# Kernel tuning notes

Measured on AMD Instinct MI355X. Metric: run time of the kernel, lower is better.

The kernel has to match this reference:

```python
import jax, jax.numpy as jnp
import numpy as np

N_TASK, N_RET, N_DRAM, N_LINK = 50000, 20000, 5000, 100000
E_RET, E_DRAM, E_LINK = 1_000_000, 250_000, 2_000_000
H = 64


def setup_inputs() -> dict:
    key = jax.random.key(0)
    k = jax.random.split(key, 17)
    s = 1.0 / np.sqrt(3 * H)
    return {
        "feat_ret":  jax.random.normal(k[0], (E_RET, 1), jnp.float32),
        "feat_dram": jax.random.normal(k[1], (E_DRAM, 1), jnp.float32),
        "feat_link": jax.random.normal(k[2], (E_LINK, 1), jnp.float32),
        "W_ret":  jax.random.normal(k[3], (H, 1), jnp.float32),
        "b_ret":  jax.random.normal(k[4], (H,), jnp.float32) * 0.1,
        "W_dram": jax.random.normal(k[5], (H, 1), jnp.float32),
        "b_dram": jax.random.normal(k[6], (H,), jnp.float32) * 0.1,
        "W_link": jax.random.normal(k[7], (H, 1), jnp.float32),
        "b_link": jax.random.normal(k[8], (H,), jnp.float32) * 0.1,
        "W_task": jax.random.normal(k[9], (H, 3 * H), jnp.float32) * s,
        "b_task": jax.random.normal(k[10], (H,), jnp.float32) * 0.1,
        "task_ret":  jax.random.randint(k[11], (E_RET,), 0, N_TASK),
        "mod_ret":   jax.random.randint(k[12], (E_RET,), 0, N_RET),
        "task_dram": jax.random.randint(k[13], (E_DRAM,), 0, N_TASK),
        "mod_dram":  jax.random.randint(k[14], (E_DRAM,), 0, N_DRAM),
        "task_link": jax.random.randint(k[15], (E_LINK,), 0, N_TASK),
        "mod_link":  jax.random.randint(k[16], (E_LINK,), 0, N_LINK),
    }


def _gather_inp(feat, mod_idx, n_mod, W, b):
    # use_X: copy_e('feat') + sum per module node, then Linear(1,H) + tanh (activate_inp)
    inp = jax.ops.segment_sum(feat, mod_idx, num_segments=n_mod)  # [n_mod, 1]
    return jnp.tanh(inp @ W.T + b)                                # [n_mod, H]


def _max_to_task(inp_mod, mod_idx, task_idx, n_task):
    # X_used_by: copy_u('inp') + max per task node; zero-in-degree tasks -> 0 (DGL convention)
    m = jax.ops.segment_max(inp_mod[mod_idx], task_idx, num_segments=n_task)
    deg = jax.ops.segment_sum(jnp.ones_like(task_idx), task_idx, num_segments=n_task)
    return jnp.where((deg > 0)[:, None], m, 0.0)


def reference(feat_ret, feat_dram, feat_link, W_ret, b_ret, W_dram, b_dram,
              W_link, b_link, W_task, b_task,
              task_ret, mod_ret, task_dram, mod_dram, task_link, mod_link):
    # _module_update_inp
    inp_ret  = _gather_inp(feat_ret,  mod_ret,  N_RET,  W_ret,  b_ret)
    inp_dram = _gather_inp(feat_dram, mod_dram, N_DRAM, W_dram, b_dram)
    inp_link = _gather_inp(feat_link, mod_link, N_LINK, W_link, b_link)

    # _task_update_h: per-etype max reduce, cross-etype concat, Linear(3H,H) + tanh
    h_cat = jnp.concatenate([
        _max_to_task(inp_ret,  mod_ret,  task_ret,  N_TASK),
        _max_to_task(inp_dram, mod_dram, task_dram, N_TASK),
        _max_to_task(inp_link, mod_link, task_link, N_TASK),
    ], axis=-1)                                                   # [N_TASK, 3H]
    h_task = jnp.tanh(h_cat @ W_task.T + b_task)                  # [N_TASK, H]

    # _module_update_h: use_link copy_u('h') + mean per link node
    s = jax.ops.segment_sum(h_task[task_link], mod_link, num_segments=N_LINK)
    deg = jax.ops.segment_sum(jnp.ones((E_LINK,), jnp.float32), mod_link, num_segments=N_LINK)
    h_link = jnp.where((deg > 0)[:, None], s / jnp.maximum(deg, 1.0)[:, None], 0.0)
    return h_link
```

## Files before the change

### kernel.cpp

```cpp
#include <hip/hip_runtime.h>
#include <stdint.h>

#define N_TASK 50000
#define N_RET 20000
#define N_DRAM 5000
#define N_LINK 100000
#define E_RET 1000000
#define E_DRAM 250000
#define E_LINK 2000000

#define SBE 4096
#define NS_RET 245
#define NS_DRAM 62
#define NS_LINK 489
#define NS_TOT (NS_RET + NS_DRAM + NS_LINK)
#define MR_RET 64
#define RSZ_RET 313
#define MR_DRAM 16
#define RSZ_DRAM 313
#define MR_LINK 256
#define RSZ_LINK 391
#define RECIP313 107203u
#define RECIP391 85817u
#define CAPM_RET 16250
#define CAPM_DRAM 16250
#define CAPM_LINK 8255
#define BM4_RET 0
#define BM4_DRAM (MR_RET * NS_RET)
#define BM4_LINK (BM4_DRAM + MR_DRAM * NS_DRAM)
#define BM4_TOT (BM4_LINK + MR_LINK * NS_LINK)
#define BT_RET 0
#define BT_DRAM (16 * NS_RET)
#define BT_LINK (BT_DRAM + 16 * NS_DRAM)
#define BT_TOT (BT_LINK + 16 * NS_LINK)

#define R_PART 3125
#define CAP_RET 63800
#define CAP_DRAM 16300
#define CAP_LINK 126800
#define SUB_RET 4
#define SUB_DRAM 1
#define SUB_LINK 8
#define PB_RET 0
#define PB_DRAM (16 * SUB_RET * R_PART)
#define PB_LINK (PB_DRAM + 16 * SUB_DRAM * R_PART)
#define PB_TOT (PB_LINK + 16 * SUB_LINK * R_PART)

#define WS_SRET 0
#define WS_SDRAM 80000
#define WS_SLINK 100000
#define WS_CNT 500000
#define WS_OFFS 900000
#define WS_TMAX 1300000
#define WS_TMIN 1900000
#define WS_BCNT 2500000
#define WS_RCNT 2500192
#define WS_CSR 2501536
#define WS_BLKM 10501536
#define WS_BLKB 11068960
#define WS_MREC_RET 15701536
#define WS_MREC_DRAM 24021536
#define WS_MREC_LINK 26101536
#define WS_PART1 15701536
#define WS_HPL0_1 20901536
#define WS_HPL1_1 24101536
#define WS_TREC32_RET 43007776
#define WS_TREC32_DRAM 47090976
#define WS_TREC32_LINK 48134176
#define WS_WTB_1 56249376
#define WS_NEED1 56273952
#define WS_PART2 10501536
#define WS_TREC_RET 15701536
#define WS_TREC_DRAM 23867936
#define WS_TREC_LINK 25954336
#define WS_HPL0_2 15701536
#define WS_HPL1_2 18901536
#define WS_WTB_2 43007776
#define WS_NEED2 43032352

typedef __attribute__((ext_vector_type(8))) short bf16x8;
typedef __attribute__((ext_vector_type(4))) float f32x4;
typedef unsigned long long u64;

__device__ __forceinline__ unsigned ford(float f) {
  unsigned u = __float_as_uint(f);
  return (u & 0x80000000u) ? ~u : (u | 0x80000000u);
}
__device__ __forceinline__ float funord(unsigned t) {
  unsigned u = (t & 0x80000000u) ? (t & 0x7fffffffu) : ~t;
  return __uint_as_float(u);
}
__device__ __forceinline__ unsigned short bf16rne(float f) {
  unsigned u = __float_as_uint(f);
  return (unsigned short)((u + 0x7fffu + ((u >> 16) & 1u)) >> 16);
}

__device__ __forceinline__ void decode_sblk(int bx, int& e, int& blk, int& E0, int& NB,
                                            int& NR, unsigned& RECIP, int& RSZ, int& base) {
  if (bx < NS_RET) {
    e = 0; blk = bx; E0 = E_RET; NB = NS_RET; NR = MR_RET; RECIP = RECIP313; RSZ = RSZ_RET; base = BM4_RET;
  } else if (bx < NS_RET + NS_DRAM) {
    e = 1; blk = bx - NS_RET; E0 = E_DRAM; NB = NS_DRAM; NR = MR_DRAM; RECIP = RECIP313; RSZ = RSZ_DRAM; base = BM4_DRAM;
  } else {
    e = 2; blk = bx - NS_RET - NS_DRAM; E0 = E_LINK; NB = NS_LINK; NR = MR_LINK; RECIP = RECIP391; RSZ = RSZ_LINK; base = BM4_LINK;
  }
}
__device__ __forceinline__ void decode_stblk(int bx, int& e, int& blk, int& E0, int& NB,
                                             int& baset) {
  if (bx < NS_RET) { e = 0; blk = bx; E0 = E_RET; NB = NS_RET; baset = BT_RET; }
  else if (bx < NS_RET + NS_DRAM) { e = 1; blk = bx - NS_RET; E0 = E_DRAM; NB = NS_DRAM; baset = BT_DRAM; }
  else { e = 2; blk = bx - NS_RET - NS_DRAM; E0 = E_LINK; NB = NS_LINK; baset = BT_LINK; }
}


__global__ __launch_bounds__(256) void k_count3(
    const int* __restrict__ mr, const int* __restrict__ md, const int* __restrict__ ml,
    const float* __restrict__ W_task, unsigned short* __restrict__ wtb,
    int* __restrict__ blkcnt_m, int* __restrict__ tcur) {
  int bx = blockIdx.x, tid = threadIdx.x;
  if (bx == NS_TOT + 48) {
    if (tid < 48) tcur[tid] = 0;
    return;
  }
  if (bx >= NS_TOT) {
    int i = (bx - NS_TOT) * 256 + tid;
    if (i < 64 * 192) wtb[i] = bf16rne(W_task[i]);
    return;
  }
  __shared__ int c[256];
  int e, blk, E0, NB, NR, RSZ, base; unsigned RECIP;
  decode_sblk(bx, e, blk, E0, NB, NR, RECIP, RSZ, base);
  const int* mod = (e == 0) ? mr : (e == 1) ? md : ml;
  c[tid] = 0;
  __syncthreads();
  int i0 = blk * SBE;
#pragma unroll
  for (int q = 0; q < 16; q++) {
    int i = i0 + q * 256 + tid;
    if (i < E0) {
      int m = mod[i];
      int r = (int)(((u64)(unsigned)m * RECIP) >> 25);
      atomicAdd(&c[r], 1);
    }
  }
  __syncthreads();
  for (int r = tid; r < NR; r += 256)
    blkcnt_m[base + r * NB + blk] = c[r];
}

__global__ __launch_bounds__(512) void k_scan3(const int* __restrict__ blkcnt_m,
                                               int* __restrict__ blkbase_m,
                                               int* __restrict__ rcnt) {
  __shared__ int sm[512];
  int gb = blockIdx.x, tid = threadIdx.x;
  int NB, off;
  if (gb < 64) { NB = NS_RET; off = BM4_RET + gb * NS_RET; }
  else if (gb < 80) { NB = NS_DRAM; off = BM4_DRAM + (gb - 64) * NS_DRAM; }
  else { NB = NS_LINK; off = BM4_LINK + (gb - 80) * NS_LINK; }
  int v = (tid < NB) ? blkcnt_m[off + tid] : 0;
  sm[tid] = v;
  __syncthreads();
  for (int d = 1; d < 512; d <<= 1) {
    int x = (tid >= d) ? sm[tid - d] : 0;
    __syncthreads();
    sm[tid] += x;
    __syncthreads();
  }
  if (tid < NB) blkbase_m[off + tid] = sm[tid] - v;
  if (tid == 511) rcnt[gb] = sm[511];
}

__global__ __launch_bounds__(512) void k_mscatter3(
    const int* __restrict__ mr, const int* __restrict__ md, const int* __restrict__ ml,
    const int* __restrict__ tr, const int* __restrict__ td, const int* __restrict__ tl,
    const float* __restrict__ fr, const float* __restrict__ fd, const float* __restrict__ fl,
    const int* __restrict__ blkcnt_m, const int* __restrict__ blkbase_m,
    u64* __restrict__ mrec_ret, u64* __restrict__ mrec_dram, u64* __restrict__ mrec_link) {
  __shared__ int lcur[256];
  __shared__ int pdelta[256];
  __shared__ int sscan[256];
  __shared__ u64 srec[SBE];
  __shared__ int sdelta[SBE];
  int tid = threadIdx.x;
  int e, blk, E0, NB, NR, RSZ, base; unsigned RECIP;
  decode_sblk(blockIdx.x, e, blk, E0, NB, NR, RECIP, RSZ, base);
  const int* mod = (e == 0) ? mr : (e == 1) ? md : ml;
  const int* task = (e == 0) ? tr : (e == 1) ? td : tl;
  const float* feat = (e == 0) ? fr : (e == 1) ? fd : fl;
  u64* out = (e == 0) ? mrec_ret : (e == 1) ? mrec_dram : mrec_link;
  int CAP = (e == 0) ? CAPM_RET : (e == 1) ? CAPM_DRAM : CAPM_LINK;
  int cnt_r = 0, base_r = 0;
  if (tid < NR) {
    cnt_r = blkcnt_m[base + tid * NB + blk];
    base_r = blkbase_m[base + tid * NB + blk];
  }
  if (tid < 256) sscan[tid] = cnt_r;
  __syncthreads();
  for (int d = 1; d < 256; d <<= 1) {
    int x = (tid < 256 && tid >= d) ? sscan[tid - d] : 0;
    __syncthreads();
    if (tid < 256) sscan[tid] += x;
    __syncthreads();
  }
  if (tid < 256) {
    int excl = sscan[tid] - cnt_r;
    lcur[tid] = excl;
    pdelta[tid] = tid * CAP + base_r - excl;
  }
  __syncthreads();
  int i0 = blk * SBE;
#pragma unroll
  for (int q = 0; q < 8; q++) {
    int i = i0 + q * 512 + tid;
    if (i < E0) {
      int m = mod[i];
      int r = (int)(((u64)(unsigned)m * RECIP) >> 25);
      unsigned mloc = (unsigned)(m - r * RSZ);
      unsigned tk = (unsigned)task[i];
      unsigned fu = __float_as_uint(feat[i]);
      int slot = atomicAdd(&lcur[r], 1);
      srec[slot] = ((u64)fu << 32) | (tk << 16) | mloc;
      int gpos = pdelta[r] + slot - r * CAP;
      sdelta[slot] = (gpos < CAP) ? pdelta[r] : (int)0x80000000;
    }
  }
  __syncthreads();
  int total = E0 - i0; if (total > SBE) total = SBE;
  for (int s = tid; s < total; s += 512) {
    int d = sdelta[s];
    if (d != (int)0x80000000) out[d + s] = srec[s];
  }
}

__global__ __launch_bounds__(1024) void k_msum3(
    const u64* __restrict__ mrec_ret, const u64* __restrict__ mrec_dram,
    const u64* __restrict__ mrec_link, const int* __restrict__ rcnt,
    int* __restrict__ cnt, int* __restrict__ offs, int* __restrict__ csr,
    int* __restrict__ tcur,
    unsigned* __restrict__ trec_ret, unsigned* __restrict__ trec_dram,
    unsigned* __restrict__ trec_link) {
  __shared__ float ssum[RSZ_LINK];
  __shared__ int scnt[RSZ_LINK];
  __shared__ int soff[RSZ_LINK + 1];
  __shared__ int red[512];
  __shared__ int tcnt16[16][16];
  __shared__ int tbase16[16][16];
  int gb = blockIdx.x, tid = threadIdx.x;
  int w = tid >> 6;
  int e, rl, RSZ, CAPM, Ntot, CAPT;
  const u64* p;
  unsigned* trec;
  if (gb < MR_RET) {
    e = 0; rl = gb; p = mrec_ret + (long)rl * CAPM_RET;
    RSZ = RSZ_RET; CAPM = CAPM_RET; Ntot = N_RET; CAPT = CAP_RET; trec = trec_ret;
  } else if (gb < MR_RET + MR_DRAM) {
    e = 1; rl = gb - MR_RET; p = mrec_dram + (long)rl * CAPM_DRAM;
    RSZ = RSZ_DRAM; CAPM = CAPM_DRAM; Ntot = N_DRAM; CAPT = CAP_DRAM; trec = trec_dram;
  } else {
    e = 2; rl = gb - MR_RET - MR_DRAM; p = mrec_link + (long)rl * CAPM_LINK;
    RSZ = RSZ_LINK; CAPM = CAPM_LINK; Ntot = N_LINK; CAPT = CAP_LINK; trec = trec_link;
  }
  int m0 = rl * RSZ;
  int nmod = Ntot - m0; if (nmod > RSZ) nmod = RSZ;
  for (int j = tid; j < RSZ; j += 1024) { ssum[j] = 0.f; scnt[j] = 0; }
  if (tid < 256) tcnt16[tid >> 4][tid & 15] = 0;
  __syncthreads();
  int count = rcnt[gb]; if (count > CAPM) count = CAPM;
  for (int i = tid; i < count; i += 1024) {
    u64 rec = p[i];
    int mloc = (int)(rec & 0xFFFFull);
    int task = (int)((rec >> 16) & 0xFFFFull);
    atomicAdd(&ssum[mloc], __uint_as_float((unsigned)(rec >> 32)));
    if (e == 2) atomicAdd(&scnt[mloc], 1);
    atomicAdd(&tcnt16[w][task / R_PART], 1);
  }
  __syncthreads();
  if (tid < 16) {
    int b2 = tid, tot = 0;
    for (int w2 = 0; w2 < 16; w2++) { tbase16[w2][b2] = tot; tot += tcnt16[w2][b2]; }
    int g0 = atomicAdd(&tcur[e * 16 + b2], tot);
    for (int w2 = 0; w2 < 16; w2++) { tbase16[w2][b2] += g0; tcnt16[w2][b2] = 0; }
  }
  if (e == 2) {
    int partial = (tid < 256 && 80 + tid < gb) ? rcnt[80 + tid] : 0;
    if (tid < 256) red[tid] = partial;
    __syncthreads();
    for (int s = 128; s > 0; s >>= 1) {
      if (tid < s) red[tid] += red[tid + s];
      __syncthreads();
    }
    int rb = red[0];
    __syncthreads();
    int vv = (tid < 512 && tid < nmod) ? scnt[tid] : 0;
    if (tid < 512) red[tid] = vv;
    __syncthreads();
    for (int d = 1; d < 512; d <<= 1) {
      int x = (tid < 512 && tid >= d) ? red[tid - d] : 0;
      __syncthreads();
      if (tid < 512) red[tid] += x;
      __syncthreads();
    }
    if (tid < nmod) soff[tid] = red[tid] - vv;
    __syncthreads();
    for (int j = tid; j < nmod; j += 1024) {
      cnt[m0 + j] = scnt[j];
      offs[m0 + j] = rb + soff[j];
    }
    __syncthreads();
    for (int i = tid; i < count; i += 1024) {
      u64 rec = p[i];
      int mloc = (int)(rec & 0xFFFFull);
      int task = (int)((rec >> 16) & 0xFFFFull);
      int lp = atomicAdd(&soff[mloc], 1);
      csr[rb + lp] = task;
    }
  }
  __syncthreads();
  for (int i = tid; i < count; i += 1024) {
    u64 rec = p[i];
    int mloc = (int)(rec & 0xFFFFull);
    int task = (int)((rec >> 16) & 0xFFFFull);
    int b = task / R_PART;
    unsigned tl12 = (unsigned)(task - b * R_PART);
    unsigned u = (ford(ssum[mloc]) & 0xFFFFF000u) | tl12;
    int local = atomicAdd(&tcnt16[w][b], 1);
    int pos = tbase16[w][b] + local;
    if (pos < CAPT) trec[(long)b * CAPT + pos] = u;
  }
}

__global__ __launch_bounds__(256) void k_passb3(
    const unsigned* __restrict__ trec_ret, const unsigned* __restrict__ trec_dram,
    const unsigned* __restrict__ trec_link,
    const int* __restrict__ tcur, unsigned* __restrict__ partials) {
  __shared__ unsigned lmax[R_PART];
  __shared__ unsigned lmin[R_PART];
  int blk = blockIdx.x;
  int e, b, sub, Nb, PB, CAP;
  const unsigned* bkt;
  if (blk < 16 * SUB_RET) {
    e = 0; b = blk >> 2; sub = blk & 3; Nb = SUB_RET; PB = PB_RET; CAP = CAP_RET; bkt = trec_ret;
  } else if (blk < 16 * (SUB_RET + SUB_DRAM)) {
    int q = blk - 16 * SUB_RET;
    e = 1; b = q; sub = 0; Nb = SUB_DRAM; PB = PB_DRAM; CAP = CAP_DRAM; bkt = trec_dram;
  } else {
    int q = blk - 16 * (SUB_RET + SUB_DRAM);
    e = 2; b = q >> 3; sub = q & 7; Nb = SUB_LINK; PB = PB_LINK; CAP = CAP_LINK; bkt = trec_link;
  }
  for (int idx = threadIdx.x; idx < R_PART; idx += 256) {
    lmax[idx] = 0u;
    lmin[idx] = 0xFFFFFFFFu;
  }
  __syncthreads();
  int count = tcur[e * 16 + b];
  if (count > CAP) count = CAP;
  int chunk = (count + Nb - 1) / Nb;
  int s0 = sub * chunk;
  int s1 = s0 + chunk; if (s1 > count) s1 = count;
  const unsigned* p = bkt + (long)b * CAP;
  for (int i = s0 + threadIdx.x; i < s1; i += 256) {
    unsigned rec = p[i];
    unsigned r = rec & 0xFFFu;
    atomicMax(&lmax[r], rec);
    atomicMin(&lmin[r], rec);
  }
  __syncthreads();
  unsigned gbase = PB + (unsigned)(b * Nb + sub) * R_PART;
  for (int idx = threadIdx.x; idx < R_PART; idx += 256) {
    partials[gbase + idx] = lmax[idx];
    partials[PB_TOT + gbase + idx] = lmin[idx];
  }
}

__global__ __launch_bounds__(256) void k_mmred3(const unsigned* __restrict__ partials,
                                                unsigned* __restrict__ tmax,
                                                unsigned* __restrict__ tmin) {
  int gid = blockIdx.x * 256 + threadIdx.x;
  if (gid >= 3 * N_TASK) return;
  int e = gid / N_TASK;
  int t = gid - e * N_TASK;
  int Nb = (e == 0) ? SUB_RET : (e == 1) ? SUB_DRAM : SUB_LINK;
  int PB = (e == 0) ? PB_RET : (e == 1) ? PB_DRAM : PB_LINK;
  int b = t / R_PART;
  int r = t - b * R_PART;
  unsigned umax = 0u, umin = 0xFFFFFFFFu;
  for (int sub = 0; sub < Nb; sub++) {
    unsigned idx = PB + (unsigned)(b * Nb + sub) * R_PART + r;
    unsigned wv = partials[idx];
    if (wv > umax) umax = wv;
    unsigned w2 = partials[PB_TOT + idx];
    if (w2 < umin) umin = w2;
  }
  tmax[gid] = umax & 0xFFFFF000u;
  tmin[gid] = umin & 0xFFFFF000u;
}


__global__ __launch_bounds__(256) void k_count(
    const int* __restrict__ mr, const int* __restrict__ md, const int* __restrict__ ml,
    const int* __restrict__ tr, const int* __restrict__ td, const int* __restrict__ tl,
    const float* __restrict__ W_task, unsigned short* __restrict__ wtb,
    int* __restrict__ blkcnt_m, int* __restrict__ blkcnt_t) {
  int bx = blockIdx.x, tid = threadIdx.x;
  if (bx >= 2 * NS_TOT) {
    int i = (bx - 2 * NS_TOT) * 256 + tid;
    if (i < 64 * 192) wtb[i] = bf16rne(W_task[i]);
    return;
  }
  __shared__ int c[256];
  c[tid] = 0;
  __syncthreads();
  if (bx < NS_TOT) {
    int e, blk, E0, NB, NR, RSZ, base; unsigned RECIP;
    decode_sblk(bx, e, blk, E0, NB, NR, RECIP, RSZ, base);
    const int* mod = (e == 0) ? mr : (e == 1) ? md : ml;
    int i0 = blk * SBE;
#pragma unroll
    for (int q = 0; q < 16; q++) {
      int i = i0 + q * 256 + tid;
      if (i < E0) {
        int m = mod[i];
        int r = (int)(((u64)(unsigned)m * RECIP) >> 25);
        atomicAdd(&c[r], 1);
      }
    }
    __syncthreads();
    for (int r = tid; r < NR; r += 256)
      blkcnt_m[base + r * NB + blk] = c[r];
  } else {
    int e, blk, E0, NB, baset;
    decode_stblk(bx - NS_TOT, e, blk, E0, NB, baset);
    const int* task = (e == 0) ? tr : (e == 1) ? td : tl;
    int i0 = blk * SBE;
#pragma unroll
    for (int q = 0; q < 16; q++) {
      int i = i0 + q * 256 + tid;
      if (i < E0) atomicAdd(&c[task[i] / R_PART], 1);
    }
    __syncthreads();
    if (tid < 16) blkcnt_t[baset + tid * NB + blk] = c[tid];
  }
}

__global__ __launch_bounds__(512) void k_scan(int* __restrict__ blkcnt_m,
                                              int* __restrict__ blkcnt_t,
                                              int* __restrict__ rcnt, int* __restrict__ bcnt) {
  __shared__ int sm[512];
  int gb = blockIdx.x, tid = threadIdx.x;
  int* arr; int NB; int* outp;
  if (gb < 336) {
    int off;
    if (gb < 64) { NB = NS_RET; off = BM4_RET + gb * NS_RET; }
    else if (gb < 80) { NB = NS_DRAM; off = BM4_DRAM + (gb - 64) * NS_DRAM; }
    else { NB = NS_LINK; off = BM4_LINK + (gb - 80) * NS_LINK; }
    arr = blkcnt_m + off; outp = rcnt + gb;
  } else {
    int g = gb - 336; int e = g >> 4, b = g & 15;
    int NBe = (e == 0) ? NS_RET : (e == 1) ? NS_DRAM : NS_LINK;
    int baset = (e == 0) ? BT_RET : (e == 1) ? BT_DRAM : BT_LINK;
    NB = NBe; arr = blkcnt_t + baset + b * NBe; outp = bcnt + g;
  }
  int v = (tid < NB) ? arr[tid] : 0;
  sm[tid] = v;
  __syncthreads();
  for (int d = 1; d < 512; d <<= 1) {
    int x = (tid >= d) ? sm[tid - d] : 0;
    __syncthreads();
    sm[tid] += x;
    __syncthreads();
  }
  if (tid < NB) arr[tid] = sm[tid] - v;
  if (tid == 511) *outp = sm[511];
}

__global__ __launch_bounds__(256) void k_mscatter2(
    const int* __restrict__ mr, const int* __restrict__ md, const int* __restrict__ ml,
    const int* __restrict__ tl,
    const float* __restrict__ fr, const float* __restrict__ fd, const float* __restrict__ fl,
    const int* __restrict__ blkcnt_m,
    u64* __restrict__ mrec_ret, u64* __restrict__ mrec_dram, u64* __restrict__ mrec_link) {
  __shared__ int lcur[256];
  __shared__ int pdelta[256];
  __shared__ int sscan[256];
  __shared__ u64 srec[SBE];
  __shared__ int sdelta[SBE];
  int tid = threadIdx.x;
  int e, blk, E0, NB, NR, RSZ, base; unsigned RECIP;
  decode_sblk(blockIdx.x, e, blk, E0, NB, NR, RECIP, RSZ, base);
  const int* mod = (e == 0) ? mr : (e == 1) ? md : ml;
  const float* feat = (e == 0) ? fr : (e == 1) ? fd : fl;
  u64* out = (e == 0) ? mrec_ret : (e == 1) ? mrec_dram : mrec_link;
  int CAP = (e == 0) ? CAPM_RET : (e == 1) ? CAPM_DRAM : CAPM_LINK;
  lcur[tid] = 0;
  __syncthreads();
  int i0 = blk * SBE;
#pragma unroll
  for (int q = 0; q < 16; q++) {
    int i = i0 + q * 256 + tid;
    if (i < E0) {
      int m = mod[i];
      int r = (int)(((u64)(unsigned)m * RECIP) >> 25);
      atomicAdd(&lcur[r], 1);
    }
  }
  __syncthreads();
  int v = lcur[tid];
  sscan[tid] = v;
  __syncthreads();
  for (int d = 1; d < 256; d <<= 1) {
    int x = (tid >= d) ? sscan[tid - d] : 0;
    __syncthreads();
    sscan[tid] += x;
    __syncthreads();
  }
  int excl = sscan[tid] - v;
  int total = sscan[255];
  int gbv = (tid < NR) ? blkcnt_m[base + tid * NB + blk] : 0;
  __syncthreads();
  lcur[tid] = excl;
  pdelta[tid] = tid * CAP + gbv - excl;
  __syncthreads();
#pragma unroll
  for (int q = 0; q < 16; q++) {
    int i = i0 + q * 256 + tid;
    if (i < E0) {
      int m = mod[i];
      int r = (int)(((u64)(unsigned)m * RECIP) >> 25);
      unsigned mloc = (unsigned)(m - r * RSZ);
      unsigned task = (e == 2) ? (unsigned)tl[i] : 0u;
      unsigned fu = __float_as_uint(feat[i]);
      int slot = atomicAdd(&lcur[r], 1);
      srec[slot] = ((u64)fu << 32) | (task << 16) | mloc;
      int gpos = pdelta[r] + slot - r * CAP;
      sdelta[slot] = (gpos < CAP) ? pdelta[r] : (int)0x80000000;
    }
  }
  __syncthreads();
  for (int s = tid; s < total; s += 256) {
    int d = sdelta[s];
    if (d != (int)0x80000000) out[d + s] = srec[s];
  }
}

__global__ __launch_bounds__(256) void k_msum(
    const u64* __restrict__ mrec_ret, const u64* __restrict__ mrec_dram,
    const u64* __restrict__ mrec_link, const int* __restrict__ rcnt,
    float* __restrict__ s_ret, float* __restrict__ s_dram, float* __restrict__ s_link,
    int* __restrict__ cnt, int* __restrict__ offs, int* __restrict__ csr) {
  __shared__ float ssum[RSZ_LINK];
  __shared__ int scnt[RSZ_LINK];
  __shared__ int soff[RSZ_LINK + 1];
  __shared__ int red[256];
  int gb = blockIdx.x, tid = threadIdx.x;
  int e, rl, RSZ, CAP, Ntot;
  const u64* p;
  float* sout;
  if (gb < MR_RET) {
    e = 0; rl = gb; p = mrec_ret + (long)rl * CAPM_RET; sout = s_ret;
    RSZ = RSZ_RET; CAP = CAPM_RET; Ntot = N_RET;
  } else if (gb < MR_RET + MR_DRAM) {
    e = 1; rl = gb - MR_RET; p = mrec_dram + (long)rl * CAPM_DRAM; sout = s_dram;
    RSZ = RSZ_DRAM; CAP = CAPM_DRAM; Ntot = N_DRAM;
  } else {
    e = 2; rl = gb - MR_RET - MR_DRAM; p = mrec_link + (long)rl * CAPM_LINK; sout = s_link;
    RSZ = RSZ_LINK; CAP = CAPM_LINK; Ntot = N_LINK;
  }
  int m0 = rl * RSZ;
  int nmod = Ntot - m0; if (nmod > RSZ) nmod = RSZ;
  for (int j = tid; j < RSZ; j += 256) { ssum[j] = 0.f; scnt[j] = 0; }
  __syncthreads();
  int count = rcnt[gb]; if (count > CAP) count = CAP;
  for (int i = tid; i < count; i += 256) {
    u64 rec = p[i];
    int mloc = (int)(rec & 0xFFFFull);
    atomicAdd(&ssum[mloc], __uint_as_float((unsigned)(rec >> 32)));
    if (e == 2) atomicAdd(&scnt[mloc], 1);
  }
  __syncthreads();
  for (int j = tid; j < nmod; j += 256) sout[m0 + j] = ssum[j];
  if (e != 2) return;
  int partial = (80 + tid < gb) ? rcnt[80 + tid] : 0;
  red[tid] = partial;
  __syncthreads();
  for (int s = 128; s > 0; s >>= 1) {
    if (tid < s) red[tid] += red[tid + s];
    __syncthreads();
  }
  int rb = red[0];
  __syncthreads();
  int a0 = (2 * tid < nmod) ? scnt[2 * tid] : 0;
  int a1 = (2 * tid + 1 < nmod) ? scnt[2 * tid + 1] : 0;
  red[tid] = a0 + a1;
  __syncthreads();
  for (int d = 1; d < 256; d <<= 1) {
    int x = (tid >= d) ? red[tid - d] : 0;
    __syncthreads();
    red[tid] += x;
    __syncthreads();
  }
  int excl = red[tid] - (a0 + a1);
  if (2 * tid < RSZ_LINK) soff[2 * tid] = excl;
  if (2 * tid + 1 < RSZ_LINK) soff[2 * tid + 1] = excl + a0;
  __syncthreads();
  for (int j = tid; j < nmod; j += 256) {
    cnt[m0 + j] = scnt[j];
    offs[m0 + j] = rb + soff[j];
  }
  __syncthreads();
  for (int i = tid; i < count; i += 256) {
    u64 rec = p[i];
    int mloc = (int)(rec & 0xFFFFull);
    int task = (int)((rec >> 16) & 0xFFFFull);
    int lp = atomicAdd(&soff[mloc], 1);
    csr[rb + lp] = task;
  }
}

__global__ __launch_bounds__(256) void k_ascatter2(
    const int* __restrict__ tr, const int* __restrict__ mr,
    const int* __restrict__ td, const int* __restrict__ md,
    const int* __restrict__ tl, const int* __restrict__ ml,
    const float* __restrict__ s_ret, const float* __restrict__ s_dram,
    const float* __restrict__ s_link, const int* __restrict__ blkcnt_t,
    u64* __restrict__ trec_ret, u64* __restrict__ trec_dram, u64* __restrict__ trec_link) {
  __shared__ int lcur[256];
  __shared__ int pdelta[256];
  __shared__ int sscan[256];
  __shared__ u64 srec[SBE];
  __shared__ int sdelta[SBE];
  int tid = threadIdx.x;
  int e, blk, E0, NB, baset;
  decode_stblk(blockIdx.x, e, blk, E0, NB, baset);
  const int* task = (e == 0) ? tr : (e == 1) ? td : tl;
  const int* mod = (e == 0) ? mr : (e == 1) ? md : ml;
  const float* s = (e == 0) ? s_ret : (e == 1) ? s_dram : s_link;
  u64* out = (e == 0) ? trec_ret : (e == 1) ? trec_dram : trec_link;
  int CAP = (e == 0) ? CAP_RET : (e == 1) ? CAP_DRAM : CAP_LINK;
  lcur[tid] = 0;
  __syncthreads();
  int i0 = blk * SBE;
#pragma unroll
  for (int q = 0; q < 16; q++) {
    int i = i0 + q * 256 + tid;
    if (i < E0) atomicAdd(&lcur[task[i] / R_PART], 1);
  }
  __syncthreads();
  int v = lcur[tid];
  sscan[tid] = v;
  __syncthreads();
  for (int d = 1; d < 256; d <<= 1) {
    int x = (tid >= d) ? sscan[tid - d] : 0;
    __syncthreads();
    sscan[tid] += x;
    __syncthreads();
  }
  int excl = sscan[tid] - v;
  int total = sscan[255];
  int gbv = (tid < 16) ? blkcnt_t[baset + tid * NB + blk] : 0;
  __syncthreads();
  lcur[tid] = excl;
  pdelta[tid] = tid * CAP + gbv - excl;
  __syncthreads();
#pragma unroll
  for (int q = 0; q < 16; q++) {
    int i = i0 + q * 256 + tid;
    if (i < E0) {
      int t = task[i];
      int r = t / R_PART;
      unsigned rloc = (unsigned)(t - r * R_PART);
      unsigned u = ford(s[mod[i]]);
      int slot = atomicAdd(&lcur[r], 1);
      srec[slot] = ((u64)u << 32) | rloc;
      int gpos = pdelta[r] + slot - r * CAP;
      sdelta[slot] = (gpos < CAP) ? pdelta[r] : (int)0x80000000;
    }
  }
  __syncthreads();
  for (int sidx = tid; sidx < total; sidx += 256) {
    int d = sdelta[sidx];
    if (d != (int)0x80000000) out[d + sidx] = srec[sidx];
  }
}

__global__ __launch_bounds__(256) void k_passb(
    const u64* __restrict__ trec_ret, const u64* __restrict__ trec_dram,
    const u64* __restrict__ trec_link,
    const int* __restrict__ bcnt, unsigned* __restrict__ partials) {
  __shared__ unsigned lmax[R_PART];
  __shared__ unsigned lmin[R_PART];
  int blk = blockIdx.x;
  int e, b, sub, Nb, PB, CAP;
  const u64* bkt;
  if (blk < 16 * SUB_RET) {
    e = 0; b = blk >> 2; sub = blk & 3; Nb = SUB_RET; PB = PB_RET; CAP = CAP_RET; bkt = trec_ret;
  } else if (blk < 16 * (SUB_RET + SUB_DRAM)) {
    int q = blk - 16 * SUB_RET;
    e = 1; b = q; sub = 0; Nb = SUB_DRAM; PB = PB_DRAM; CAP = CAP_DRAM; bkt = trec_dram;
  } else {
    int q = blk - 16 * (SUB_RET + SUB_DRAM);
    e = 2; b = q >> 3; sub = q & 7; Nb = SUB_LINK; PB = PB_LINK; CAP = CAP_LINK; bkt = trec_link;
  }
  for (int idx = threadIdx.x; idx < R_PART; idx += 256) {
    lmax[idx] = 0u;
    lmin[idx] = 0xFFFFFFFFu;
  }
  __syncthreads();
  int count = bcnt[e * 16 + b];
  if (count > CAP) count = CAP;
  int chunk = (count + Nb - 1) / Nb;
  int s0 = sub * chunk;
  int s1 = s0 + chunk; if (s1 > count) s1 = count;
  const u64* p = bkt + (long)b * CAP;
  for (int i = s0 + threadIdx.x; i < s1; i += 256) {
    u64 rec = p[i];
    unsigned r = (unsigned)rec;
    unsigned u = (unsigned)(rec >> 32);
    atomicMax(&lmax[r], u);
    atomicMin(&lmin[r], u);
  }
  __syncthreads();
  unsigned gbase = PB + (unsigned)(b * Nb + sub) * R_PART;
  for (int idx = threadIdx.x; idx < R_PART; idx += 256) {
    partials[gbase + idx] = lmax[idx];
    partials[PB_TOT + gbase + idx] = lmin[idx];
  }
}

__global__ __launch_bounds__(256) void k_mmred2(const unsigned* __restrict__ partials,
                                                unsigned* __restrict__ tmax,
                                                unsigned* __restrict__ tmin) {
  int gid = blockIdx.x * 256 + threadIdx.x;
  if (gid >= 3 * N_TASK) return;
  int e = gid / N_TASK;
  int t = gid - e * N_TASK;
  int Nb = (e == 0) ? SUB_RET : (e == 1) ? SUB_DRAM : SUB_LINK;
  int PB = (e == 0) ? PB_RET : (e == 1) ? PB_DRAM : PB_LINK;
  int b = t / R_PART;
  int r = t - b * R_PART;
  unsigned umax = 0u, umin = 0xFFFFFFFFu;
  for (int sub = 0; sub < Nb; sub++) {
    unsigned idx = PB + (unsigned)(b * Nb + sub) * R_PART + r;
    unsigned wv = partials[idx];
    if (wv > umax) umax = wv;
    unsigned w2 = partials[PB_TOT + idx];
    if (w2 < umin) umin = w2;
  }
  tmax[gid] = umax;
  tmin[gid] = umin;
}


__global__ void k_wprep(const float* __restrict__ W_task, unsigned short* __restrict__ wtb) {
  int i = blockIdx.x * 256 + threadIdx.x;
  if (i < 64 * 192) wtb[i] = bf16rne(W_task[i]);
}

__global__ void f_segsum(const float* __restrict__ fr, const float* __restrict__ fd,
                         const float* __restrict__ fl,
                         const int* __restrict__ mr, const int* __restrict__ md,
                         const int* __restrict__ ml,
                         float* s_ret, float* s_dram, float* s_link, int* cnt) {
  int i = blockIdx.x * blockDim.x + threadIdx.x;
  const int total = E_RET + E_DRAM + E_LINK;
  if (i >= total) return;
  if (i < E_RET) {
    atomicAdd(&s_ret[mr[i]], fr[i]);
  } else if (i < E_RET + E_DRAM) {
    int j = i - E_RET;
    atomicAdd(&s_dram[md[j]], fd[j]);
  } else {
    int j = i - (E_RET + E_DRAM);
    int m = ml[j];
    atomicAdd(&s_link[m], fl[j]);
    atomicAdd(&cnt[m], 1);
  }
}

__global__ void f_minmax(const float* __restrict__ s_ret, const float* __restrict__ s_dram,
                         const float* __restrict__ s_link,
                         const int* __restrict__ tr, const int* __restrict__ mr,
                         const int* __restrict__ td, const int* __restrict__ md,
                         const int* __restrict__ tl, const int* __restrict__ ml,
                         unsigned* tmax, unsigned* tmin) {
  int i = blockIdx.x * blockDim.x + threadIdx.x;
  const int total = E_RET + E_DRAM + E_LINK;
  if (i >= total) return;
  int e, task; unsigned u;
  if (i < E_RET) {
    u = ford(s_ret[mr[i]]); task = tr[i]; e = 0;
  } else if (i < E_RET + E_DRAM) {
    int j = i - E_RET;
    u = ford(s_dram[md[j]]); task = td[j]; e = 1;
  } else {
    int j = i - (E_RET + E_DRAM);
    u = ford(s_link[ml[j]]); task = tl[j]; e = 2;
  }
  atomicMax(&tmax[e * N_TASK + task], u);
  atomicMin(&tmin[e * N_TASK + task], u);
}

__global__ void f_part(const int* __restrict__ cnt, int* part) {
  __shared__ int sm[256];
  int i = blockIdx.x * 256 + threadIdx.x;
  sm[threadIdx.x] = (i < N_LINK) ? cnt[i] : 0;
  __syncthreads();
  for (int s = 128; s > 0; s >>= 1) {
    if (threadIdx.x < s) sm[threadIdx.x] += sm[threadIdx.x + s];
    __syncthreads();
  }
  if (threadIdx.x == 0) part[blockIdx.x] = sm[0];
}

__global__ void f_scanpart(const int* __restrict__ part, int* partx, int npart) {
  __shared__ int sm[512];
  int t = threadIdx.x;
  int v = (t < npart) ? part[t] : 0;
  sm[t] = v;
  __syncthreads();
  for (int d = 1; d < 512; d <<= 1) {
    int x = (t >= d) ? sm[t - d] : 0;
    __syncthreads();
    sm[t] += x;
    __syncthreads();
  }
  if (t < npart) partx[t] = sm[t] - v;
}

__global__ void f_offs(const int* __restrict__ cnt, const int* __restrict__ partx,
                       int* offs, int* cursor) {
  __shared__ int sm[256];
  int i = blockIdx.x * 256 + threadIdx.x;
  int t = threadIdx.x;
  int v = (i < N_LINK) ? cnt[i] : 0;
  sm[t] = v;
  __syncthreads();
  for (int d = 1; d < 256; d <<= 1) {
    int x = (t >= d) ? sm[t - d] : 0;
    __syncthreads();
    sm[t] += x;
    __syncthreads();
  }
  if (i < N_LINK) {
    int o = partx[blockIdx.x] + sm[t] - v;
    offs[i] = o;
    cursor[i] = o;
  }
}

__global__ void f_scatter(const int* __restrict__ tl, const int* __restrict__ ml,
                          int* cursor, int* csr) {
  int i = blockIdx.x * blockDim.x + threadIdx.x;
  if (i >= E_LINK) return;
  int pos = atomicAdd(&cursor[ml[i]], 1);
  csr[pos] = tl[i];
}


__global__ __launch_bounds__(256) void k_taskm(
    const float* __restrict__ W_ret, const float* __restrict__ b_ret,
    const float* __restrict__ W_dram, const float* __restrict__ b_dram,
    const float* __restrict__ W_link, const float* __restrict__ b_link,
    const unsigned short* __restrict__ wtb, const float* __restrict__ b_task,
    const unsigned* __restrict__ tmax, const unsigned* __restrict__ tmin,
    unsigned short* __restrict__ hp0, unsigned short* __restrict__ hp1) {
  int wave = threadIdx.x >> 6;
  int lane = threadIdx.x & 63;
  int tile = blockIdx.x * 4 + wave;
  if (tile >= N_TASK / 16) return;
  int t0 = tile * 16;
  int l16 = lane & 15;
  int quad = lane >> 4;
  int t = t0 + l16;

  f32x4 acc[4];
#pragma unroll
  for (int nf = 0; nf < 4; nf++) acc[nf] = (f32x4){0.f, 0.f, 0.f, 0.f};

  const float* We[3] = {W_ret, W_dram, W_link};
  const float* be[3] = {b_ret, b_dram, b_link};

  for (int e = 0; e < 3; e++) {
    unsigned um = tmax[e * N_TASK + t];
    float smax = funord(um);
    float smin = funord(tmin[e * N_TASK + t]);
    bool live = (um != 0u);
#pragma unroll
    for (int h = 0; h < 2; h++) {
      int kb = h * 32 + quad * 8;
      float4 w0 = *(const float4*)&We[e][kb];
      float4 w1 = *(const float4*)&We[e][kb + 4];
      float4 b0 = *(const float4*)&be[e][kb];
      float4 b1 = *(const float4*)&be[e][kb + 4];
      float wv[8] = {w0.x, w0.y, w0.z, w0.w, w1.x, w1.y, w1.z, w1.w};
      float bv[8] = {b0.x, b0.y, b0.z, b0.w, b1.x, b1.y, b1.z, b1.w};
      bf16x8 afrag;
#pragma unroll
      for (int j = 0; j < 8; j++) {
        float wj = wv[j];
        float ss = (wj >= 0.f) ? smax : smin;
        float hc = live ? tanhf(fmaf(ss, wj, bv[j])) : 0.f;
        afrag[j] = (short)bf16rne(hc);
      }
      int kk = e * 64 + h * 32 + quad * 8;
#pragma unroll
      for (int nf = 0; nf < 4; nf++) {
        int o = nf * 16 + l16;
        bf16x8 bfrag = *(const bf16x8*)&wtb[o * 192 + kk];
        acc[nf] = __builtin_amdgcn_mfma_f32_16x16x32_bf16(afrag, bfrag, acc[nf], 0, 0, 0);
      }
    }
  }

#pragma unroll
  for (int nf = 0; nf < 4; nf++) {
    int n = nf * 16 + l16;
    float bt = b_task[n];
    unsigned short* hp = (n < 32) ? hp0 : hp1;
    int f = n & 31;
#pragma unroll
    for (int r = 0; r < 4; r++) {
      int m = quad * 4 + r;
      float v = tanhf(acc[nf][r] + bt);
      hp[(t0 + m) * 32 + f] = bf16rne(v);
    }
  }
}

__global__ __launch_bounds__(256) void k_link2(const unsigned short* __restrict__ hp,
                                               const int* __restrict__ offs,
                                               const int* __restrict__ cnt,
                                               const int* __restrict__ csr,
                                               float* __restrict__ out, int plane) {
  int l = blockIdx.x * 8 + (threadIdx.x >> 5);
  int f = threadIdx.x & 31;
  int start = offs[l];
  int c = cnt[l];
  float acc = 0.f;
  for (int q = 0; q < c; q += 4) {
    int i1 = (q + 1 < c) ? q + 1 : c - 1;
    int i2 = (q + 2 < c) ? q + 2 : c - 1;
    int i3 = (q + 3 < c) ? q + 3 : c - 1;
    int t0 = csr[start + q];
    int t1 = csr[start + i1];
    int t2 = csr[start + i2];
    int t3 = csr[start + i3];
    unsigned v0 = hp[t0 * 32 + f];
    unsigned v1 = hp[t1 * 32 + f];
    unsigned v2 = hp[t2 * 32 + f];
    unsigned v3 = hp[t3 * 32 + f];
    acc += __uint_as_float(v0 << 16);
    if (q + 1 < c) acc += __uint_as_float(v1 << 16);
    if (q + 2 < c) acc += __uint_as_float(v2 << 16);
    if (q + 3 < c) acc += __uint_as_float(v3 << 16);
  }
  out[l * 64 + plane * 32 + f] = (c > 0) ? acc / (float)c : 0.f;
}

extern "C" void kernel_launch(void* const* d_in, const int* in_sizes, int n_in,
                              void* d_out, int out_size, void* d_ws, size_t ws_size,
                              hipStream_t stream) {
  const float* feat_ret  = (const float*)d_in[0];
  const float* feat_dram = (const float*)d_in[1];
  const float* feat_link = (const float*)d_in[2];
  const float* W_ret  = (const float*)d_in[3];
  const float* b_ret  = (const float*)d_in[4];
  const float* W_dram = (const float*)d_in[5];
  const float* b_dram = (const float*)d_in[6];
  const float* W_link = (const float*)d_in[7];
  const float* b_link = (const float*)d_in[8];
  const float* W_task = (const float*)d_in[9];
  const float* b_task = (const float*)d_in[10];
  const int* task_ret  = (const int*)d_in[11];
  const int* mod_ret   = (const int*)d_in[12];
  const int* task_dram = (const int*)d_in[13];
  const int* mod_dram  = (const int*)d_in[14];
  const int* task_link = (const int*)d_in[15];
  const int* mod_link  = (const int*)d_in[16];
  float* out = (float*)d_out;

  char* ws = (char*)d_ws;
  float* s_ret  = (float*)(ws + WS_SRET);
  float* s_dram = (float*)(ws + WS_SDRAM);
  float* s_link = (float*)(ws + WS_SLINK);
  int*   cnt    = (int*)(ws + WS_CNT);
  int*   offs   = (int*)(ws + WS_OFFS);
  unsigned* tmax = (unsigned*)(ws + WS_TMAX);
  unsigned* tmin = (unsigned*)(ws + WS_TMIN);
  int* tcur = (int*)(ws + WS_BCNT);
  int* rcnt = (int*)(ws + WS_RCNT);
  int* csr  = (int*)(ws + WS_CSR);
  int* blkcnt_m = (int*)(ws + WS_BLKM);
  int* blkb = (int*)(ws + WS_BLKB);
  u64* mrec_ret  = (u64*)(ws + WS_MREC_RET);
  u64* mrec_dram = (u64*)(ws + WS_MREC_DRAM);
  u64* mrec_link = (u64*)(ws + WS_MREC_LINK);

  unsigned short* hp0;
  unsigned short* hp1;
  unsigned short* wtb;

  if (ws_size >= (size_t)WS_NEED1) {
    unsigned* partials = (unsigned*)(ws + WS_PART1);
    unsigned* trec_ret  = (unsigned*)(ws + WS_TREC32_RET);
    unsigned* trec_dram = (unsigned*)(ws + WS_TREC32_DRAM);
    unsigned* trec_link = (unsigned*)(ws + WS_TREC32_LINK);
    hp0 = (unsigned short*)(ws + WS_HPL0_1);
    hp1 = (unsigned short*)(ws + WS_HPL1_1);
    wtb = (unsigned short*)(ws + WS_WTB_1);
    k_count3<<<NS_TOT + 49, 256, 0, stream>>>(mod_ret, mod_dram, mod_link,
                                              W_task, wtb, blkcnt_m, tcur);
    k_scan3<<<336, 512, 0, stream>>>(blkcnt_m, blkb, rcnt);
    k_mscatter3<<<NS_TOT, 512, 0, stream>>>(mod_ret, mod_dram, mod_link,
                                            task_ret, task_dram, task_link,
                                            feat_ret, feat_dram, feat_link,
                                            blkcnt_m, blkb,
                                            mrec_ret, mrec_dram, mrec_link);
    k_msum3<<<336, 1024, 0, stream>>>(mrec_ret, mrec_dram, mrec_link, rcnt,
                                      cnt, offs, csr, tcur,
                                      trec_ret, trec_dram, trec_link);
    k_passb3<<<16 * (SUB_RET + SUB_DRAM + SUB_LINK), 256, 0, stream>>>(
        trec_ret, trec_dram, trec_link, tcur, partials);
    k_mmred3<<<(3 * N_TASK + 255) / 256, 256, 0, stream>>>(partials, tmax, tmin);
  } else if (ws_size >= (size_t)WS_NEED2) {
    unsigned* partials = (unsigned*)(ws + WS_PART2);
    u64* trec_ret  = (u64*)(ws + WS_TREC_RET);
    u64* trec_dram = (u64*)(ws + WS_TREC_DRAM);
    u64* trec_link = (u64*)(ws + WS_TREC_LINK);
    hp0 = (unsigned short*)(ws + WS_HPL0_2);
    hp1 = (unsigned short*)(ws + WS_HPL1_2);
    wtb = (unsigned short*)(ws + WS_WTB_2);
    k_count<<<2 * NS_TOT + 48, 256, 0, stream>>>(mod_ret, mod_dram, mod_link,
                                                 task_ret, task_dram, task_link,
                                                 W_task, wtb, blkcnt_m, blkb);
    k_scan<<<384, 512, 0, stream>>>(blkcnt_m, blkb, rcnt, tcur);
    k_mscatter2<<<NS_TOT, 256, 0, stream>>>(mod_ret, mod_dram, mod_link, task_link,
                                            feat_ret, feat_dram, feat_link, blkcnt_m,
                                            mrec_ret, mrec_dram, mrec_link);
    k_msum<<<336, 256, 0, stream>>>(mrec_ret, mrec_dram, mrec_link, rcnt,
                                    s_ret, s_dram, s_link, cnt, offs, csr);
    k_ascatter2<<<NS_TOT, 256, 0, stream>>>(task_ret, mod_ret, task_dram, mod_dram,
                                            task_link, mod_link, s_ret, s_dram, s_link,
                                            blkb, trec_ret, trec_dram, trec_link);
    k_passb<<<16 * (SUB_RET + SUB_DRAM + SUB_LINK), 256, 0, stream>>>(
        trec_ret, trec_dram, trec_link, tcur, partials);
    k_mmred2<<<(3 * N_TASK + 255) / 256, 256, 0, stream>>>(partials, tmax, tmin);
  } else {
    int* part   = (int*)(ws + WS_BLKM);
    int* partx  = (int*)(ws + WS_BLKM + 4096);
    int* cursor = (int*)(ws + WS_BLKB);
    hp0 = (unsigned short*)(ws + WS_HPL0_2);
    hp1 = (unsigned short*)(ws + WS_HPL1_2);
    wtb = (unsigned short*)(ws + WS_WTB_2);
    hipMemsetAsync(ws, 0, 1900000, stream);
    hipMemsetAsync(ws + WS_TMIN, 0xFF, 600000, stream);
    const int totalE = E_RET + E_DRAM + E_LINK;
    int nblk_e = (totalE + 255) / 256;
    f_segsum<<<nblk_e, 256, 0, stream>>>(feat_ret, feat_dram, feat_link,
                                         mod_ret, mod_dram, mod_link,
                                         s_ret, s_dram, s_link, cnt);
    f_minmax<<<nblk_e, 256, 0, stream>>>(s_ret, s_dram, s_link,
                                         task_ret, mod_ret, task_dram, mod_dram,
                                         task_link, mod_link, tmax, tmin);
    const int npart = (N_LINK + 255) / 256;
    f_part<<<npart, 256, 0, stream>>>(cnt, part);
    f_scanpart<<<1, 512, 0, stream>>>(part, partx, npart);
    f_offs<<<npart, 256, 0, stream>>>(cnt, partx, offs, cursor);
    f_scatter<<<(E_LINK + 255) / 256, 256, 0, stream>>>(task_link, mod_link, cursor, csr);
    k_wprep<<<48, 256, 0, stream>>>(W_task, wtb);
  }

  k_taskm<<<(N_TASK / 16 + 3) / 4, 256, 0, stream>>>(W_ret, b_ret, W_dram, b_dram,
                                                     W_link, b_link, wtb, b_task,
                                                     tmax, tmin, hp0, hp1);
  k_link2<<<N_LINK / 8, 256, 0, stream>>>(hp0, offs, cnt, csr, out, 0);
  k_link2<<<N_LINK / 8, 256, 0, stream>>>(hp1, offs, cnt, csr, out, 1);
}
```

Before: 312.6 us.

## Merge link region pairs per msum block, fuse CSR scatter, unroll loops

k_msum3 now handles two link module regions per block, so the grid shrinks from 336 to 208 blocks, and the prefix scan widens to 1024 entries. The CSR scatter pass is folded into the trec emission loop, which removes one full reread of the records and one barrier. Both record loops and the passb loop are unrolled by four so several independent loads are in flight, and k_passb3 moves to 1024-thread blocks. The aim is lower launch and reread overhead plus more memory-level parallelism, at the cost of fewer blocks for the link portion and extra LDS use.

```diff
diff --git a/kernel.cpp b/kernel.cpp
--- a/kernel.cpp
+++ b/kernel.cpp
@@ -232,6 +232,24 @@
   }
 }
 
+#define P1BODY(rec, moff) { \
+  int mloc_ = (int)((rec) & 0xFFFFull) + (moff); \
+  int task_ = (int)(((rec) >> 16) & 0xFFFFull); \
+  atomicAdd(&ssum[mloc_], __uint_as_float((unsigned)((rec) >> 32))); \
+  if (e == 2) atomicAdd(&scnt[mloc_], 1); \
+  atomicAdd(&tcnt16[w][task_ / R_PART], 1); }
+
+#define P3BODY(rec, moff) { \
+  int mloc_ = (int)((rec) & 0xFFFFull) + (moff); \
+  int task_ = (int)(((rec) >> 16) & 0xFFFFull); \
+  if (e == 2) { int lp_ = atomicAdd(&soff[mloc_], 1); csr[rb + lp_] = task_; } \
+  int b_ = task_ / R_PART; \
+  unsigned tl12_ = (unsigned)(task_ - b_ * R_PART); \
+  unsigned u_ = (ford(ssum[mloc_]) & 0xFFFFF000u) | tl12_; \
+  int local_ = atomicAdd(&tcnt16[w][b_], 1); \
+  int pos_ = tbase16[w][b_] + local_; \
+  if (pos_ < CAPT) trec[(long)b_ * CAPT + pos_] = u_; }
+
 __global__ __launch_bounds__(1024) void k_msum3(
     const u64* __restrict__ mrec_ret, const u64* __restrict__ mrec_dram,
     const u64* __restrict__ mrec_link, const int* __restrict__ rcnt,
@@ -239,40 +257,55 @@
     int* __restrict__ tcur,
     unsigned* __restrict__ trec_ret, unsigned* __restrict__ trec_dram,
     unsigned* __restrict__ trec_link) {
-  __shared__ float ssum[RSZ_LINK];
-  __shared__ int scnt[RSZ_LINK];
-  __shared__ int soff[RSZ_LINK + 1];
-  __shared__ int red[512];
+  __shared__ float ssum[2 * RSZ_LINK];
+  __shared__ int scnt[2 * RSZ_LINK];
+  __shared__ int soff[2 * RSZ_LINK + 1];
+  __shared__ int red[1024];
   __shared__ int tcnt16[16][16];
   __shared__ int tbase16[16][16];
   int gb = blockIdx.x, tid = threadIdx.x;
   int w = tid >> 6;
-  int e, rl, RSZ, CAPM, Ntot, CAPT;
-  const u64* p;
+  int e, m0, nmod, RSZtot, CAPT, rl0 = 0;
+  int cnt0, cnt1 = 0;
+  const u64 *p0, *p1 = nullptr;
   unsigned* trec;
   if (gb < MR_RET) {
-    e = 0; rl = gb; p = mrec_ret + (long)rl * CAPM_RET;
-    RSZ = RSZ_RET; CAPM = CAPM_RET; Ntot = N_RET; CAPT = CAP_RET; trec = trec_ret;
+    e = 0; p0 = mrec_ret + (long)gb * CAPM_RET;
+    cnt0 = rcnt[gb]; if (cnt0 > CAPM_RET) cnt0 = CAPM_RET;
+    RSZtot = RSZ_RET; m0 = gb * RSZ_RET; nmod = N_RET - m0;
+    CAPT = CAP_RET; trec = trec_ret;
   } else if (gb < MR_RET + MR_DRAM) {
-    e = 1; rl = gb - MR_RET; p = mrec_dram + (long)rl * CAPM_DRAM;
-    RSZ = RSZ_DRAM; CAPM = CAPM_DRAM; Ntot = N_DRAM; CAPT = CAP_DRAM; trec = trec_dram;
+    e = 1; int rl = gb - MR_RET; p0 = mrec_dram + (long)rl * CAPM_DRAM;
+    cnt0 = rcnt[gb]; if (cnt0 > CAPM_DRAM) cnt0 = CAPM_DRAM;
+    RSZtot = RSZ_DRAM; m0 = rl * RSZ_DRAM; nmod = N_DRAM - m0;
+    CAPT = CAP_DRAM; trec = trec_dram;
   } else {
-    e = 2; rl = gb - MR_RET - MR_DRAM; p = mrec_link + (long)rl * CAPM_LINK;
-    RSZ = RSZ_LINK; CAPM = CAPM_LINK; Ntot = N_LINK; CAPT = CAP_LINK; trec = trec_link;
-  }
-  int m0 = rl * RSZ;
-  int nmod = Ntot - m0; if (nmod > RSZ) nmod = RSZ;
-  for (int j = tid; j < RSZ; j += 1024) { ssum[j] = 0.f; scnt[j] = 0; }
+    e = 2; rl0 = 2 * (gb - (MR_RET + MR_DRAM));
+    p0 = mrec_link + (long)rl0 * CAPM_LINK; p1 = p0 + CAPM_LINK;
+    cnt0 = rcnt[80 + rl0]; if (cnt0 > CAPM_LINK) cnt0 = CAPM_LINK;
+    cnt1 = rcnt[80 + rl0 + 1]; if (cnt1 > CAPM_LINK) cnt1 = CAPM_LINK;
+    RSZtot = 2 * RSZ_LINK; m0 = rl0 * RSZ_LINK; nmod = N_LINK - m0;
+    CAPT = CAP_LINK; trec = trec_link;
+  }
+  if (nmod > RSZtot) nmod = RSZtot;
+  for (int j = tid; j < RSZtot; j += 1024) { ssum[j] = 0.f; scnt[j] = 0; }
   if (tid < 256) tcnt16[tid >> 4][tid & 15] = 0;
   __syncthreads();
-  int count = rcnt[gb]; if (count > CAPM) count = CAPM;
-  for (int i = tid; i < count; i += 1024) {
-    u64 rec = p[i];
-    int mloc = (int)(rec & 0xFFFFull);
-    int task = (int)((rec >> 16) & 0xFFFFull);
-    atomicAdd(&ssum[mloc], __uint_as_float((unsigned)(rec >> 32)));
-    if (e == 2) atomicAdd(&scnt[mloc], 1);
-    atomicAdd(&tcnt16[w][task / R_PART], 1);
+  {
+    int i = tid;
+    for (; i + 3072 < cnt0; i += 4096) {
+      u64 a = p0[i], b = p0[i + 1024], c = p0[i + 2048], d = p0[i + 3072];
+      P1BODY(a, 0) P1BODY(b, 0) P1BODY(c, 0) P1BODY(d, 0)
+    }
+    for (; i < cnt0; i += 1024) { u64 a = p0[i]; P1BODY(a, 0) }
+    if (e == 2) {
+      i = tid;
+      for (; i + 3072 < cnt1; i += 4096) {
+        u64 a = p1[i], b = p1[i + 1024], c = p1[i + 2048], d = p1[i + 3072];
+        P1BODY(a, RSZ_LINK) P1BODY(b, RSZ_LINK) P1BODY(c, RSZ_LINK) P1BODY(d, RSZ_LINK)
+      }
+      for (; i < cnt1; i += 1024) { u64 a = p1[i]; P1BODY(a, RSZ_LINK) }
+    }
   }
   __syncthreads();
   if (tid < 16) {
@@ -281,23 +314,24 @@
     int g0 = atomicAdd(&tcur[e * 16 + b2], tot);
     for (int w2 = 0; w2 < 16; w2++) { tbase16[w2][b2] += g0; tcnt16[w2][b2] = 0; }
   }
+  int rb = 0;
   if (e == 2) {
-    int partial = (tid < 256 && 80 + tid < gb) ? rcnt[80 + tid] : 0;
+    int partial = (tid < 256 && tid < rl0) ? rcnt[80 + tid] : 0;
     if (tid < 256) red[tid] = partial;
     __syncthreads();
     for (int s = 128; s > 0; s >>= 1) {
       if (tid < s) red[tid] += red[tid + s];
       __syncthreads();
     }
-    int rb = red[0];
-    __syncthreads();
-    int vv = (tid < 512 && tid < nmod) ? scnt[tid] : 0;
-    if (tid < 512) red[tid] = vv;
-    __syncthreads();
-    for (int d = 1; d < 512; d <<= 1) {
-      int x = (tid < 512 && tid >= d) ? red[tid - d] : 0;
+    rb = red[0];
+    __syncthreads();
+    int vv = (tid < nmod) ? scnt[tid] : 0;
+    red[tid] = vv;
+    __syncthreads();
+    for (int d = 1; d < 1024; d <<= 1) {
+      int x = (tid >= d) ? red[tid - d] : 0;
       __syncthreads();
-      if (tid < 512) red[tid] += x;
+      red[tid] += x;
       __syncthreads();
     }
     if (tid < nmod) soff[tid] = red[tid] - vv;
@@ -306,36 +340,40 @@
       cnt[m0 + j] = scnt[j];
       offs[m0 + j] = rb + soff[j];
     }
-    __syncthreads();
-    for (int i = tid; i < count; i += 1024) {
-      u64 rec = p[i];
-      int mloc = (int)(rec & 0xFFFFull);
-      int task = (int)((rec >> 16) & 0xFFFFull);
-      int lp = atomicAdd(&soff[mloc], 1);
-      csr[rb + lp] = task;
-    }
-  }
-  __syncthreads();
-  for (int i = tid; i < count; i += 1024) {
-    u64 rec = p[i];
-    int mloc = (int)(rec & 0xFFFFull);
-    int task = (int)((rec >> 16) & 0xFFFFull);
-    int b = task / R_PART;
-    unsigned tl12 = (unsigned)(task - b * R_PART);
-    unsigned u = (ford(ssum[mloc]) & 0xFFFFF000u) | tl12;
-    int local = atomicAdd(&tcnt16[w][b], 1);
-    int pos = tbase16[w][b] + local;
-    if (pos < CAPT) trec[(long)b * CAPT + pos] = u;
-  }
-}
-
-__global__ __launch_bounds__(256) void k_passb3(
+  }
+  __syncthreads();
+  {
+    int i = tid;
+    for (; i + 3072 < cnt0; i += 4096) {
+      u64 a = p0[i], b = p0[i + 1024], c = p0[i + 2048], d = p0[i + 3072];
+      P3BODY(a, 0) P3BODY(b, 0) P3BODY(c, 0) P3BODY(d, 0)
+    }
+    for (; i < cnt0; i += 1024) { u64 a = p0[i]; P3BODY(a, 0) }
+    if (e == 2) {
+      i = tid;
+      for (; i + 3072 < cnt1; i += 4096) {
+        u64 a = p1[i], b = p1[i + 1024], c = p1[i + 2048], d = p1[i + 3072];
+        P3BODY(a, RSZ_LINK) P3BODY(b, RSZ_LINK) P3BODY(c, RSZ_LINK) P3BODY(d, RSZ_LINK)
+      }
+      for (; i < cnt1; i += 1024) { u64 a = p1[i]; P3BODY(a, RSZ_LINK) }
+    }
+  }
+}
+#undef P1BODY
+#undef P3BODY
+
+#define PBBODY(rec) { \
+  unsigned r_ = (rec) & 0xFFFu; \
+  atomicMax(&lmax[r_], (rec)); \
+  atomicMin(&lmin[r_], (rec)); }
+
+__global__ __launch_bounds__(1024) void k_passb3(
     const unsigned* __restrict__ trec_ret, const unsigned* __restrict__ trec_dram,
     const unsigned* __restrict__ trec_link,
     const int* __restrict__ tcur, unsigned* __restrict__ partials) {
   __shared__ unsigned lmax[R_PART];
   __shared__ unsigned lmin[R_PART];
-  int blk = blockIdx.x;
+  int blk = blockIdx.x, tid = threadIdx.x;
   int e, b, sub, Nb, PB, CAP;
   const unsigned* bkt;
   if (blk < 16 * SUB_RET) {
@@ -347,7 +385,7 @@
     int q = blk - 16 * (SUB_RET + SUB_DRAM);
     e = 2; b = q >> 3; sub = q & 7; Nb = SUB_LINK; PB = PB_LINK; CAP = CAP_LINK; bkt = trec_link;
   }
-  for (int idx = threadIdx.x; idx < R_PART; idx += 256) {
+  for (int idx = tid; idx < R_PART; idx += 1024) {
     lmax[idx] = 0u;
     lmin[idx] = 0xFFFFFFFFu;
   }
@@ -358,19 +396,20 @@
   int s0 = sub * chunk;
   int s1 = s0 + chunk; if (s1 > count) s1 = count;
   const unsigned* p = bkt + (long)b * CAP;
-  for (int i = s0 + threadIdx.x; i < s1; i += 256) {
-    unsigned rec = p[i];
-    unsigned r = rec & 0xFFFu;
-    atomicMax(&lmax[r], rec);
-    atomicMin(&lmin[r], rec);
-  }
+  int i = s0 + tid;
+  for (; i + 3072 < s1; i += 4096) {
+    unsigned r0 = p[i], r1 = p[i + 1024], r2 = p[i + 2048], r3 = p[i + 3072];
+    PBBODY(r0) PBBODY(r1) PBBODY(r2) PBBODY(r3)
+  }
+  for (; i < s1; i += 1024) { unsigned r0 = p[i]; PBBODY(r0) }
   __syncthreads();
   unsigned gbase = PB + (unsigned)(b * Nb + sub) * R_PART;
-  for (int idx = threadIdx.x; idx < R_PART; idx += 256) {
+  for (int idx = tid; idx < R_PART; idx += 1024) {
     partials[gbase + idx] = lmax[idx];
     partials[PB_TOT + gbase + idx] = lmin[idx];
   }
 }
+#undef PBBODY
 
 __global__ __launch_bounds__(256) void k_mmred3(const unsigned* __restrict__ partials,
                                                 unsigned* __restrict__ tmax,
@@ -1015,10 +1054,11 @@
                                             feat_ret, feat_dram, feat_link,
                                             blkcnt_m, blkb,
                                             mrec_ret, mrec_dram, mrec_link);
-    k_msum3<<<336, 1024, 0, stream>>>(mrec_ret, mrec_dram, mrec_link, rcnt,
-                                      cnt, offs, csr, tcur,
-                                      trec_ret, trec_dram, trec_link);
-    k_passb3<<<16 * (SUB_RET + SUB_DRAM + SUB_LINK), 256, 0, stream>>>(
+    k_msum3<<<MR_RET + MR_DRAM + MR_LINK / 2, 1024, 0, stream>>>(
+        mrec_ret, mrec_dram, mrec_link, rcnt,
+        cnt, offs, csr, tcur,
+        trec_ret, trec_dram, trec_link);
+    k_passb3<<<16 * (SUB_RET + SUB_DRAM + SUB_LINK), 1024, 0, stream>>>(
         trec_ret, trec_dram, trec_link, tcur, partials);
     k_mmred3<<<(3 * N_TASK + 255) / 256, 256, 0, stream>>>(partials, tmax, tmin);
   } else if (ws_size >= (size_t)WS_NEED2) {
```

Measured after the change: 293.7 us. 1.06x faster.
